# Performance work log

Measured on AMD Instinct MI355X. Metric: run time of the kernel, lower is better.

Reference implementation:

```python
import jax, jax.numpy as jnp
import numpy as np

DIM = 1024
HEADS = 16
HEAD_DIM = DIM // HEADS
EPS = 1e-5


def setup_inputs() -> dict:
    key = jax.random.key(0)
    ks = jax.random.split(key, 4)
    N, L = 4, 2048
    x = jax.random.normal(ks[0], (N, L, DIM), dtype=jnp.float32)
    # causal mask: True means masked (strictly upper triangle)
    attn_mask = jnp.triu(jnp.ones((L, L), dtype=jnp.bool_), k=1)[None, None, :, :]
    w_qkv = jax.random.normal(ks[1], (3 * DIM, DIM), dtype=jnp.float32) * (DIM ** -0.5)
    w_proj = jax.random.normal(ks[2], (DIM, DIM), dtype=jnp.float32) * (DIM ** -0.5)
    b_proj = jnp.zeros((DIM,), dtype=jnp.float32)
    q_gamma = jnp.ones((HEAD_DIM,), dtype=jnp.float32)
    q_beta = jnp.zeros((HEAD_DIM,), dtype=jnp.float32)
    k_gamma = jnp.ones((HEAD_DIM,), dtype=jnp.float32)
    k_beta = jnp.zeros((HEAD_DIM,), dtype=jnp.float32)
    return {"x": x, "attn_mask": attn_mask, "w_qkv": w_qkv, "w_proj": w_proj,
            "b_proj": b_proj, "q_gamma": q_gamma, "q_beta": q_beta,
            "k_gamma": k_gamma, "k_beta": k_beta}


def _layernorm(h, gamma, beta):
    mu = jnp.mean(h, axis=-1, keepdims=True)
    var = jnp.mean(jnp.square(h - mu), axis=-1, keepdims=True)
    return (h - mu) * jax.lax.rsqrt(var + EPS) * gamma + beta


def reference(x, attn_mask, w_qkv, w_proj, b_proj, q_gamma, q_beta, k_gamma, k_beta):
    N, L, D = x.shape
    H, hd = HEADS, HEAD_DIM
    scale = hd ** -0.5
    qkv = jnp.einsum('nld,ed->nle', x, w_qkv)  # [N, L, 3D]
    qkv = qkv.reshape(N, L, 3, H, hd).transpose(2, 0, 3, 1, 4)  # [3, N, H, L, hd]
    q, k, v = qkv[0], qkv[1], qkv[2]
    q = _layernorm(q, q_gamma, q_beta)
    k = _layernorm(k, k_gamma, k_beta)
    scores = jnp.einsum('nhqd,nhkd->nhqk', q * scale, k)
    scores = scores + jnp.where(attn_mask, -jnp.inf, 0.0).astype(scores.dtype)
    attn = jax.nn.softmax(scores, axis=-1)
    out = jnp.einsum('nhqk,nhkd->nhqd', attn, v)  # [N, H, L, hd]
    out = out.transpose(0, 2, 1, 3).reshape(N, L, D)
    return jnp.einsum('nld,ed->nle', out, w_proj) + b_proj
```

## Files before the change

kernel.cpp:

```cpp
#include <hip/hip_runtime.h>


using f16x8 = __attribute__((ext_vector_type(8))) _Float16;
using f16x4 = __attribute__((ext_vector_type(4))) _Float16;
using f16x2 = __attribute__((ext_vector_type(2))) _Float16;
using f32x4 = __attribute__((ext_vector_type(4))) float;
using f32x16 = __attribute__((ext_vector_type(16))) float;
using u32x4 = __attribute__((ext_vector_type(4))) unsigned int;

#define MFMA16(a, b, c) __builtin_amdgcn_mfma_f32_16x16x32_f16(a, b, c, 0, 0, 0)
#define MFMA32(a, b, c) __builtin_amdgcn_mfma_f32_32x32x16_f16(a, b, c, 0, 0, 0)

__device__ __forceinline__ void gload_lds16(const void* g, void* l) {
  __builtin_amdgcn_global_load_lds(
      (const __attribute__((address_space(1))) unsigned int*)g,
      (__attribute__((address_space(3))) unsigned int*)l, 16, 0, 0);
}

__device__ __forceinline__ float dot2acc(unsigned int pk, float c) {
#if __has_builtin(__builtin_amdgcn_fdot2)
  const f16x2 ones = {(_Float16)1.f, (_Float16)1.f};
  return __builtin_amdgcn_fdot2(__builtin_bit_cast(f16x2, pk), ones, c, false);
#else
  f16x2 v = __builtin_bit_cast(f16x2, pk);
  return c + (float)v[0] + (float)v[1];
#endif
}

__global__ __launch_bounds__(256) void convert_all_kernel(
    const float* __restrict__ x, const float* __restrict__ wq,
    const float* __restrict__ wp, _Float16* __restrict__ xb,
    _Float16* __restrict__ wqb, _Float16* __restrict__ wpb) {
  long i = ((long)blockIdx.x * 256 + threadIdx.x) * 8;
  const float* src;
  _Float16* dst;
  if (i < 8388608) {
    src = x; dst = xb;
  } else if (i < 8388608 + 3145728) {
    src = wq + (i - 8388608); dst = wqb + (i - 8388608); i = 0;
  } else {
    src = wp + (i - 11534336); dst = wpb + (i - 11534336); i = 0;
  }
  float4 a = *(const float4*)(src + i);
  float4 b = *(const float4*)(src + i + 4);
  f16x8 o;
  o[0] = (_Float16)a.x; o[1] = (_Float16)a.y; o[2] = (_Float16)a.z; o[3] = (_Float16)a.w;
  o[4] = (_Float16)b.x; o[5] = (_Float16)b.y; o[6] = (_Float16)b.z; o[7] = (_Float16)b.w;
  *(f16x8*)(dst + i) = o;
}

template <int MODE>
__global__ __launch_bounds__(256, 3) void gemm_bt(
    const _Float16* __restrict__ A, const _Float16* __restrict__ B,
    void* __restrict__ Cout, _Float16* __restrict__ Vt,
    const float* __restrict__ bias,
    const float* __restrict__ qg, const float* __restrict__ qb,
    const float* __restrict__ kg, const float* __restrict__ kb,
    int M, int N, int K) {
  __shared__ __align__(16) char smem[49152];
  const int tid = threadIdx.x;
  const int w = tid >> 6, lane = tid & 63;
  const int c = lane & 15, g = lane >> 4;
  const long mbase = (long)blockIdx.x * 128;
  const int by = (MODE == 1) ? (int)((blockIdx.y + 16) % 24) : (int)blockIdx.y;
  const long nbase = (long)by * 128;
  const int wm = (w >> 1) * 64, wn = (w & 1) * 64;
  const int sr4 = lane >> 2;
  const int scol = ((lane & 3) ^ ((lane >> 3) & 3)) * 8;
  const int sg = (g ^ ((c >> 1) & 3)) * 8;
  const char* pAr = smem + (wm + c) * 64 + sg * 2;
  const char* pBr = smem + 24576 + (wn + c) * 64 + sg * 2;

#define GSTAGE(off_, kt_)                                                     \
  {                                                                           \
    const int kk_ = (kt_) * 32;                                               \
    _Pragma("unroll") for (int i = 0; i < 2; ++i) {                           \
      const int arow = w * 32 + i * 16 + sr4;                                 \
      gload_lds16(A + (mbase + arow) * K + kk_ + scol,                        \
                  smem + (off_) + (w * 2 + i) * 1024);                        \
    }                                                                         \
    _Pragma("unroll") for (int j = 0; j < 2; ++j) {                           \
      const int brow = w * 32 + j * 16 + sr4;                                 \
      gload_lds16(B + (nbase + brow) * K + kk_ + scol,                        \
                  smem + 24576 + (off_) + (w * 2 + j) * 1024);                \
    }                                                                         \
  }

  f32x4 acc[4][4];
#pragma unroll
  for (int i = 0; i < 4; ++i)
#pragma unroll
    for (int j = 0; j < 4; ++j) acc[i][j] = f32x4{0.f, 0.f, 0.f, 0.f};

  const int nk = K >> 5;
  GSTAGE(0, 0);
  GSTAGE(8192, 1);
  int rOff = 0, sOff = 16384;
  for (int kt = 0; kt < nk; ++kt) {
    if (kt + 1 < nk) {
      asm volatile("s_waitcnt vmcnt(4)" ::: "memory");
    } else {
      asm volatile("s_waitcnt vmcnt(0)" ::: "memory");
    }
    __builtin_amdgcn_sched_barrier(0);
    __builtin_amdgcn_s_barrier();
    __builtin_amdgcn_sched_barrier(0);
    f16x8 af[4], bfr[4];
#pragma unroll
    for (int mt = 0; mt < 4; ++mt)
      af[mt] = *(const f16x8*)(pAr + rOff + mt * 1024);
#pragma unroll
    for (int nt = 0; nt < 4; ++nt)
      bfr[nt] = *(const f16x8*)(pBr + rOff + nt * 1024);
    if (kt + 2 < nk) GSTAGE(sOff, kt + 2);
#pragma unroll
    for (int mt = 0; mt < 4; ++mt)
#pragma unroll
      for (int nt = 0; nt < 4; ++nt)
        acc[mt][nt] = MFMA16(af[mt], bfr[nt], acc[mt][nt]);
    rOff = (rOff == 16384) ? 0 : rOff + 8192;
    sOff = (sOff == 16384) ? 0 : sOff + 8192;
  }
#undef GSTAGE

  if constexpr (MODE == 1) {
    const int region = by >> 3;
    if (region == 2) {
      __syncthreads();
      _Float16* T = (_Float16*)smem;
#pragma unroll
      for (int nt = 0; nt < 4; ++nt) {
        const int dloc = wn + nt * 16 + c;
#pragma unroll
        for (int mt = 0; mt < 4; ++mt) {
          const int lloc = wm + mt * 16 + g * 4;
          f16x4 o;
#pragma unroll
          for (int r = 0; r < 4; ++r) o[r] = (_Float16)acc[mt][nt][r];
          *(f16x4*)(T + dloc * 136 + lloc) = o;
        }
      }
      __syncthreads();
      const long n = mbase >> 11;
      const long lbase = mbase & 2047;
      const int chunk = tid & 15;
      const int rbase = tid >> 4;
#pragma unroll
      for (int i = 0; i < 8; ++i) {
        const int row = rbase + i * 16;
        const long dcol = (nbase - 2048) + row;
        *(f16x8*)(Vt + (n * 1024 + dcol) * 2048 + lbase + chunk * 8) =
            *(const f16x8*)(T + row * 136 + chunk * 8);
      }
      return;
    }
    const float* gamma = region ? kg : qg;
    const float* beta = region ? kb : qb;
    float gam[4], bet[4];
#pragma unroll
    for (int nt = 0; nt < 4; ++nt) {
      gam[nt] = gamma[nt * 16 + c];
      bet[nt] = beta[nt * 16 + c];
    }
    const float sc = region ? 1.f : 0.1803368801111204f;
#pragma unroll
    for (int mt = 0; mt < 4; ++mt)
#pragma unroll
      for (int r = 0; r < 4; ++r) {
        float s1 = 0.f, s2 = 0.f;
#pragma unroll
        for (int nt = 0; nt < 4; ++nt) {
          const float v = acc[mt][nt][r];
          s1 += v;
          s2 += v * v;
        }
#pragma unroll
        for (int msk = 1; msk < 16; msk <<= 1) {
          s1 += __shfl_xor(s1, msk);
          s2 += __shfl_xor(s2, msk);
        }
        const float mu = s1 * 0.015625f;
        const float rstd = rsqrtf(s2 * 0.015625f - mu * mu + 1e-5f);
#pragma unroll
        for (int nt = 0; nt < 4; ++nt)
          acc[mt][nt][r] =
              ((acc[mt][nt][r] - mu) * rstd * gam[nt] + bet[nt]) * sc;
      }
#pragma unroll
    for (int nt = 0; nt < 4; ++nt) {
      const long col = nbase + wn + nt * 16 + c;
#pragma unroll
      for (int mt = 0; mt < 4; ++mt)
#pragma unroll
        for (int r = 0; r < 4; ++r) {
          const long row = mbase + wm + mt * 16 + g * 4 + r;
          ((_Float16*)Cout)[row * N + col] = (_Float16)acc[mt][nt][r];
        }
    }
  } else {
#pragma unroll
    for (int nt = 0; nt < 4; ++nt) {
      const long col = nbase + wn + nt * 16 + c;
      const float bv = bias ? bias[col] : 0.f;
#pragma unroll
      for (int mt = 0; mt < 4; ++mt)
#pragma unroll
        for (int r = 0; r < 4; ++r) {
          const long row = mbase + wm + mt * 16 + g * 4 + r;
          ((float*)Cout)[row * N + col] = acc[mt][nt][r] + bv;
        }
    }
  }
}

__global__ __launch_bounds__(256, 4) void attn_kernel(
    const _Float16* __restrict__ qkv, const _Float16* __restrict__ Vt,
    _Float16* __restrict__ Ob) {
  __shared__ __align__(16) char lds[32768];
  const int w = threadIdx.x >> 6;
  const int lane = threadIdx.x & 63;
  const int c5 = lane & 31;
  const int hi = lane >> 5;
  const int lin = (int)(blockIdx.x + 64 * blockIdx.y);
  const int nh = (lin & 7) * 8 + ((lin >> 3) & 7);
  const long n = nh >> 4;
  const int h = nh & 15;
  const int qtile = 15 - (lin >> 6);
  const int qlo_blk = qtile * 128;
  const int qlo = qlo_blk + w * 32;
  const int qrow = qlo + c5;

  const _Float16* Qp = qkv + n * 2048 * 3072 + h * 64;
  const _Float16* Kq = Qp + 1024;
  const _Float16* Vp = Vt + (long)nh * 64 * 2048;

  const int sr8 = lane >> 3;
  const int scol = ((lane & 7) ^ sr8) * 8;

  const int nkv_blk = (qlo_blk + 191) >> 6;
  const int nkv_w = (qlo + 95) >> 6;

#define STAGE(BUF, kv_)                                                        \
  {                                                                            \
    const int kb_ = (kv_) * 64;                                                \
    _Pragma("unroll") for (int i = 0; i < 2; ++i) {                            \
      const int idx = w * 2 + i;                                               \
      const int row = idx * 8 + sr8;                                           \
      gload_lds16(Kq + (long)(kb_ + row) * 3072 + scol,                        \
                  lds + (BUF) * 8192 + idx * 1024);                            \
      gload_lds16(Vp + (long)row * 2048 + kb_ + scol,                          \
                  lds + 16384 + (BUF) * 8192 + idx * 1024);                    \
    }                                                                          \
  }

  f16x8 qf[4];
#pragma unroll
  for (int dc = 0; dc < 4; ++dc)
    qf[dc] = *(const f16x8*)(Qp + (long)qrow * 3072 + dc * 16 + hi * 8);

  f32x16 negM;
#pragma unroll
  for (int r = 0; r < 16; ++r) negM[r] = -12.0f;

  f32x16 acc[2];
#pragma unroll
  for (int db = 0; db < 2; ++db)
#pragma unroll
    for (int r = 0; r < 16; ++r) acc[db][r] = 0.f;
  float ls = 0.f;

  const int swr = c5 & 7;
  const char* Lb[4];
#pragma unroll
  for (int j = 0; j < 4; ++j)
    Lb[j] = lds + c5 * 128 + (((j * 2 + hi) ^ swr) << 4);

#define COMPUTE(BUF, kv_)                                                      \
  {                                                                            \
    const int kbase = (kv_) * 64;                                              \
    f32x16 s0, s1;                                                             \
    __builtin_amdgcn_s_setprio(1);                                             \
    {                                                                          \
      f16x8 kf0 = *(const f16x8*)(Lb[0] + (BUF) * 8192);                       \
      f16x8 kf1 = *(const f16x8*)(Lb[0] + (BUF) * 8192 + 4096);                \
      s0 = MFMA32(kf0, qf[0], negM);                                           \
      s1 = MFMA32(kf1, qf[0], negM);                                           \
    }                                                                          \
    _Pragma("unroll") for (int dc = 1; dc < 4; ++dc) {                         \
      f16x8 kf0 = *(const f16x8*)(Lb[dc] + (BUF) * 8192);                      \
      f16x8 kf1 = *(const f16x8*)(Lb[dc] + (BUF) * 8192 + 4096);               \
      s0 = MFMA32(kf0, qf[dc], s0);                                            \
      s1 = MFMA32(kf1, qf[dc], s1);                                            \
    }                                                                          \
    __builtin_amdgcn_s_setprio(0);                                             \
    if (kbase + 63 > qlo) {                                                    \
      _Pragma("unroll") for (int r = 0; r < 16; ++r) {                         \
        const int mv = (r & 3) + 8 * (r >> 2) + 4 * hi;                        \
        if (kbase + mv > qrow) s0[r] = -1e30f;                                 \
        if (kbase + 32 + mv > qrow) s1[r] = -1e30f;                            \
      }                                                                        \
    }                                                                          \
    _Pragma("unroll") for (int r = 0; r < 16; ++r) {                           \
      s0[r] = exp2f(s0[r]);                                                    \
      s1[r] = exp2f(s1[r]);                                                    \
    }                                                                          \
    unsigned int pk0[4][2], pk1[4][2];                                         \
    _Pragma("unroll") for (int r2 = 0; r2 < 4; ++r2)                           \
        _Pragma("unroll") for (int p = 0; p < 2; ++p) {                        \
      pk0[r2][p] = __builtin_bit_cast(                                         \
          unsigned int, __builtin_amdgcn_cvt_pkrtz(s0[4 * r2 + 2 * p],         \
                                                   s0[4 * r2 + 2 * p + 1]));   \
      pk1[r2][p] = __builtin_bit_cast(                                         \
          unsigned int, __builtin_amdgcn_cvt_pkrtz(s1[4 * r2 + 2 * p],         \
                                                   s1[4 * r2 + 2 * p + 1]));   \
    }                                                                          \
    _Pragma("unroll") for (int r2 = 0; r2 < 4; ++r2)                           \
        _Pragma("unroll") for (int p = 0; p < 2; ++p) {                        \
      ls = dot2acc(pk0[r2][p], ls);                                            \
      ls = dot2acc(pk1[r2][p], ls);                                            \
    }                                                                          \
    f16x8 pB[4];                                                               \
    _Pragma("unroll") for (int kk = 0; kk < 4; ++kk) {                         \
      const int rx = (kk & 1) * 2;                                             \
      unsigned int x0 = (kk < 2) ? pk0[rx][0] : pk1[rx][0];                    \
      unsigned int y0 = (kk < 2) ? pk0[rx + 1][0] : pk1[rx + 1][0];            \
      unsigned int x1 = (kk < 2) ? pk0[rx][1] : pk1[rx][1];                    \
      unsigned int y1 = (kk < 2) ? pk0[rx + 1][1] : pk1[rx + 1][1];            \
      asm("v_permlane32_swap_b32 %0, %1" : "+v"(x0), "+v"(y0));                \
      asm("v_permlane32_swap_b32 %0, %1" : "+v"(x1), "+v"(y1));                \
      pB[kk] = __builtin_bit_cast(f16x8, u32x4{x0, x1, y0, y1});               \
    }                                                                          \
    __builtin_amdgcn_s_setprio(1);                                             \
    _Pragma("unroll") for (int db = 0; db < 2; ++db)                           \
        _Pragma("unroll") for (int kk = 0; kk < 4; ++kk) {                     \
      f16x8 vf = *(const f16x8*)(Lb[kk] + 16384 + (BUF) * 8192 + db * 4096);   \
      acc[db] = MFMA32(vf, pB[kk], acc[db]);                                   \
    }                                                                          \
    __builtin_amdgcn_s_setprio(0);                                             \
  }

  STAGE(0, 0);
  for (int kv = 0; kv < nkv_blk; kv += 2) {
    __syncthreads();
    if (kv + 1 < nkv_blk) STAGE(1, kv + 1);
    if (kv < nkv_w) COMPUTE(0, kv);
    if (kv + 1 >= nkv_blk) break;
    __syncthreads();
    if (kv + 2 < nkv_blk) STAGE(0, kv + 2);
    if (kv + 1 < nkv_w) COMPUTE(1, kv + 1);
  }
#undef COMPUTE
#undef STAGE

  const float lsr = ls + __shfl_xor(ls, 32);
  const float inv = 1.f / lsr;
  _Float16* ob = Ob + ((long)(n * 2048) + qrow) * 1024 + h * 64 + 4 * hi;
#pragma unroll
  for (int db = 0; db < 2; ++db)
#pragma unroll
    for (int r2 = 0; r2 < 4; ++r2) {
      f16x4 o;
#pragma unroll
      for (int j = 0; j < 4; ++j)
        o[j] = (_Float16)(acc[db][4 * r2 + j] * inv);
      *(f16x4*)(ob + db * 32 + 8 * r2) = o;
    }
}

extern "C" void kernel_launch(void* const* d_in, const int* in_sizes, int n_in,
                              void* d_out, int out_size, void* d_ws, size_t ws_size,
                              hipStream_t stream) {
  const float* x = (const float*)d_in[0];
  const float* w_qkv = (const float*)d_in[2];
  const float* w_proj = (const float*)d_in[3];
  const float* b_proj = (const float*)d_in[4];
  const float* qg = (const float*)d_in[5];
  const float* qb = (const float*)d_in[6];
  const float* kg = (const float*)d_in[7];
  const float* kb = (const float*)d_in[8];

  char* ws = (char*)d_ws;
  _Float16* xb     = (_Float16*)(ws + 0);
  _Float16* wqkvb  = (_Float16*)(ws + 16777216);
  _Float16* wprojb = (_Float16*)(ws + 23068672);
  _Float16* qkvh   = (_Float16*)(ws + 25165824);
  _Float16* Vt     = (_Float16*)(ws + 75497472);
  _Float16* Ob     = xb;

  convert_all_kernel<<<6144, 256, 0, stream>>>(x, w_qkv, w_proj,
                                               xb, wqkvb, wprojb);

  gemm_bt<1><<<dim3(64, 24), 256, 0, stream>>>(xb, wqkvb, qkvh, Vt, nullptr,
                                               qg, qb, kg, kb, 8192, 3072, 1024);
  attn_kernel<<<dim3(64, 16), 256, 0, stream>>>(qkvh, Vt, Ob);
  gemm_bt<0><<<dim3(64, 8), 256, 0, stream>>>(Ob, wprojb, d_out, nullptr, b_proj,
                                              nullptr, nullptr, nullptr, nullptr,
                                              8192, 1024, 1024);
}
```

Before: 187.5 us.

## Triple-buffer KV tiles in attention with partial vmcnt waits

Moves the attention kernel's K/V staging from double buffering to a three-slot ring in LDS (48KB) and prefetches two tiles ahead. Each iteration waits with a partial vmcnt count and a single barrier, so global-to-LDS loads overlap more with compute. The cost is more LDS per block: launch bounds drop from 4 to 3 blocks per CU, which lowers occupancy, and the code now depends on a manually counted vmcnt.

```diff
diff --git a/kernel.cpp b/kernel.cpp
--- a/kernel.cpp
+++ b/kernel.cpp
@@ -213,10 +213,10 @@
   }
 }
 
-__global__ __launch_bounds__(256, 4) void attn_kernel(
+__global__ __launch_bounds__(256, 3) void attn_kernel(
     const _Float16* __restrict__ qkv, const _Float16* __restrict__ Vt,
     _Float16* __restrict__ Ob) {
-  __shared__ __align__(16) char lds[32768];
+  __shared__ __align__(16) char lds[49152];
   const int w = threadIdx.x >> 6;
   const int lane = threadIdx.x & 63;
   const int c5 = lane & 31;
@@ -240,16 +240,16 @@
   const int nkv_blk = (qlo_blk + 191) >> 6;
   const int nkv_w = (qlo + 95) >> 6;
 
-#define STAGE(BUF, kv_)                                                        \
+#define STAGE(OFF, kv_)                                                        \
   {                                                                            \
     const int kb_ = (kv_) * 64;                                                \
     _Pragma("unroll") for (int i = 0; i < 2; ++i) {                            \
       const int idx = w * 2 + i;                                               \
       const int row = idx * 8 + sr8;                                           \
       gload_lds16(Kq + (long)(kb_ + row) * 3072 + scol,                        \
-                  lds + (BUF) * 8192 + idx * 1024);                            \
+                  lds + (OFF) + idx * 1024);                                   \
       gload_lds16(Vp + (long)row * 2048 + kb_ + scol,                          \
-                  lds + 16384 + (BUF) * 8192 + idx * 1024);                    \
+                  lds + (OFF) + 8192 + idx * 1024);                            \
     }                                                                          \
   }
 
@@ -275,20 +275,20 @@
   for (int j = 0; j < 4; ++j)
     Lb[j] = lds + c5 * 128 + (((j * 2 + hi) ^ swr) << 4);
 
-#define COMPUTE(BUF, kv_)                                                      \
+#define COMPUTE(OFF, kv_)                                                      \
   {                                                                            \
     const int kbase = (kv_) * 64;                                              \
     f32x16 s0, s1;                                                             \
     __builtin_amdgcn_s_setprio(1);                                             \
     {                                                                          \
-      f16x8 kf0 = *(const f16x8*)(Lb[0] + (BUF) * 8192);                       \
-      f16x8 kf1 = *(const f16x8*)(Lb[0] + (BUF) * 8192 + 4096);                \
+      f16x8 kf0 = *(const f16x8*)(Lb[0] + (OFF));                              \
+      f16x8 kf1 = *(const f16x8*)(Lb[0] + (OFF) + 4096);                       \
       s0 = MFMA32(kf0, qf[0], negM);                                           \
       s1 = MFMA32(kf1, qf[0], negM);                                           \
     }                                                                          \
     _Pragma("unroll") for (int dc = 1; dc < 4; ++dc) {                         \
-      f16x8 kf0 = *(const f16x8*)(Lb[dc] + (BUF) * 8192);                      \
-      f16x8 kf1 = *(const f16x8*)(Lb[dc] + (BUF) * 8192 + 4096);               \
+      f16x8 kf0 = *(const f16x8*)(Lb[dc] + (OFF));                             \
+      f16x8 kf1 = *(const f16x8*)(Lb[dc] + (OFF) + 4096);                      \
       s0 = MFMA32(kf0, qf[dc], s0);                                            \
       s1 = MFMA32(kf1, qf[dc], s1);                                            \
     }                                                                          \
@@ -333,21 +333,28 @@
     __builtin_amdgcn_s_setprio(1);                                             \
     _Pragma("unroll") for (int db = 0; db < 2; ++db)                           \
         _Pragma("unroll") for (int kk = 0; kk < 4; ++kk) {                     \
-      f16x8 vf = *(const f16x8*)(Lb[kk] + 16384 + (BUF) * 8192 + db * 4096);   \
+      f16x8 vf = *(const f16x8*)(Lb[kk] + (OFF) + 8192 + db * 4096);           \
       acc[db] = MFMA32(vf, pB[kk], acc[db]);                                   \
     }                                                                          \
     __builtin_amdgcn_s_setprio(0);                                             \
   }
 
   STAGE(0, 0);
-  for (int kv = 0; kv < nkv_blk; kv += 2) {
-    __syncthreads();
-    if (kv + 1 < nkv_blk) STAGE(1, kv + 1);
-    if (kv < nkv_w) COMPUTE(0, kv);
-    if (kv + 1 >= nkv_blk) break;
-    __syncthreads();
-    if (kv + 2 < nkv_blk) STAGE(0, kv + 2);
-    if (kv + 1 < nkv_w) COMPUTE(1, kv + 1);
+  STAGE(16384, 1);
+  int rOff = 0, sOff = 32768;
+  for (int kv = 0; kv < nkv_blk; ++kv) {
+    if (kv + 1 < nkv_blk) {
+      asm volatile("s_waitcnt vmcnt(4)" ::: "memory");
+    } else {
+      asm volatile("s_waitcnt vmcnt(0)" ::: "memory");
+    }
+    __builtin_amdgcn_sched_barrier(0);
+    __builtin_amdgcn_s_barrier();
+    __builtin_amdgcn_sched_barrier(0);
+    if (kv + 2 < nkv_blk) STAGE(sOff, kv + 2);
+    if (kv < nkv_w) COMPUTE(rOff, kv);
+    rOff = (rOff == 32768) ? 0 : rOff + 16384;
+    sOff = (sOff == 32768) ? 0 : sOff + 16384;
   }
 #undef COMPUTE
 #undef STAGE
```

New measurement: 186.3 us (median of 3 runs). No clear change (-0.6%).
